# Optimization experiments

Measured on AMD Instinct MI355X. Metric: run time of the kernel, lower is better.

The kernel has to match this reference:

```python
import jax, jax.numpy as jnp
import numpy as np

B, N, D, DEG = 16, 8192, 384, 16
K, H, STEPS = 8, 128, 3


def setup_inputs() -> dict:
    key = jax.random.key(0)
    ks = jax.random.split(key, 8)
    s_in = 1.0 / np.sqrt(2 * D)
    s_h = 1.0 / np.sqrt(H)
    return {
        "q_embs": jax.random.normal(ks[0], (B, D), jnp.float32),
        "emb": jax.random.normal(ks[1], (B, N, D), jnp.float32),
        "neighbors": jax.random.randint(ks[2], (B, N, DEG), 0, N, jnp.int32),
        "labels": jax.random.randint(ks[3], (B, N), 0, 2, jnp.int32),
        "W1": jax.random.normal(ks[4], (2 * D, H), jnp.float32) * s_in,
        "b1": jnp.zeros((H,), jnp.float32),
        "W2": jax.random.normal(ks[5], (H, K), jnp.float32) * s_h,
        "b2": jnp.zeros((K,), jnp.float32),
        "P1": jax.random.normal(ks[6], (2 * D, H), jnp.float32) * s_in,
        "pb1": jnp.zeros((H,), jnp.float32),
        "P2": jax.random.normal(ks[7], (H, 1), jnp.float32) * s_h,
        "pb2": jnp.zeros((1,), jnp.float32),
    }


def reference(q_embs, emb, neighbors, labels, W1, b1, W2, b2, P1, pb1, P2, pb2):
    b, n, d = emb.shape
    k = W2.shape[1]
    # inp = [emb | q broadcast]  -> [B, N, 2D]
    inp = jnp.concatenate([emb, jnp.broadcast_to(q_embs[:, None, :], emb.shape)], axis=-1)
    # path_net: sigmoid(MLP) -> [B, N], then +1 at support (label==1) nodes
    path = jax.nn.sigmoid(jax.nn.relu(inp @ P1 + pb1) @ P2 + pb2)[..., 0]
    path = path + labels.astype(path.dtype)
    # coin_net amplitudes scaled by (1 + path)
    amps = (jax.nn.relu(inp @ W1 + b1) @ W2 + b2) * (1.0 + path)[..., None]  # [B,N,K]
    # initial uniform state
    state = jnp.full((b, n, k), 1.0 / np.sqrt(n * k), dtype=emb.dtype)

    # sparse adjacency diffusion: out[i] = sum_{j in nbrs[i]} st[j]
    spmm = jax.vmap(lambda st, nb: st[nb].sum(axis=1))  # st [N,K], nb [N,DEG]

    for _ in range(STEPS):
        st = spmm(state * amps, neighbors)                 # [B,N,K]
        norm = jnp.linalg.norm(st.reshape(b, -1), axis=1)[:, None, None]
        state = jnp.where(norm > 0, st / norm, st)
    return jnp.abs(state).sum(axis=-1)  # [B,N]
```

## Files before the change

kernel.cpp:

```cpp
#include <hip/hip_runtime.h>
#include <cstdint>
#include <cstddef>

#define BB 16
#define NN 8192
#define DD 384
#define HH 128
#define KK 8
#define DEG 16

typedef short bf8_t __attribute__((ext_vector_type(8)));
typedef float f4_t __attribute__((ext_vector_type(4)));

__device__ __forceinline__ unsigned short f2bf(float f) {
  unsigned int u = __float_as_uint(f);
  u += 0x7FFFu + ((u >> 16) & 1u);
  return (unsigned short)(u >> 16);
}

__global__ __launch_bounds__(256) void kprep(
    const float* __restrict__ q, const float* __restrict__ W1,
    const float* __restrict__ b1, const float* __restrict__ P1,
    const float* __restrict__ pb1,
    unsigned short* __restrict__ W1t, unsigned short* __restrict__ P1t,
    float* __restrict__ base1, float* __restrict__ baseP,
    float* __restrict__ normsq)
{
  int blk = blockIdx.x, t = threadIdx.x;
  if (blk < BB) {
    int net = t >> 7, h = t & 127;
    const float* W = net ? P1 : W1;
    float acc = net ? pb1[h] : b1[h];
    const float* qb = q + blk * DD;
    for (int d = 0; d < DD; ++d)
      acc = fmaf(qb[d], W[(DD + d) * HH + h], acc);
    (net ? baseP : base1)[blk * HH + h] = acc;
  } else {
    int e = (blk - BB) * 3072 + t;
    for (int it = 0; it < 12; ++it, e += 256) {
      int net = e / 49152;
      int r = e - net * 49152;
      int d = r >> 7;
      int h = r & 127;
      float v = (net ? P1 : W1)[d * HH + h];
      (net ? P1t : W1t)[h * DD + d] = f2bf(v);
    }
    if (blk == BB && t < BB) normsq[t] = 0.f;
  }
}

__global__ __launch_bounds__(256) void kmlp(
    const float* __restrict__ emb, const int* __restrict__ labels,
    const unsigned short* __restrict__ W1t, const unsigned short* __restrict__ P1t,
    const float* __restrict__ base1, const float* __restrict__ baseP,
    const float* __restrict__ W2, const float* __restrict__ b2,
    const float* __restrict__ P2, const float* __restrict__ pb2,
    float* __restrict__ amps)
{
  __shared__ __align__(16) unsigned short sA[64 * 40];
  __shared__ __align__(16) unsigned short sB1[128 * 40];
  __shared__ __align__(16) unsigned short sBP[128 * 40];
  __shared__ float sBase1[128], sBaseP[128], sW2t[8 * 128], sP2[128], sB2[8];

  const int t = threadIdx.x;
  const int b = blockIdx.x >> 7;
  const int row0 = (blockIdx.x & 127) * 64;
  const int gbase = b * NN + row0;

  if (t < 128) { sBase1[t] = base1[b * HH + t]; sP2[t] = P2[t]; }
  else         { sBaseP[t - 128] = baseP[b * HH + (t - 128)]; }
  for (int e = t; e < HH * KK; e += 256) {
    int h = e >> 3, kk = e & 7;
    sW2t[kk * 128 + h] = W2[e];
  }
  if (t < 8) sB2[t] = b2[t];

  const int w = t >> 6, lane = t & 63, q = lane >> 4, ln = lane & 15;
  f4_t zero = {0.f, 0.f, 0.f, 0.f};
  f4_t acc1[8], accP[8];
#pragma unroll
  for (int i = 0; i < 8; ++i) { acc1[i] = zero; accP[i] = zero; }

  const int ar = t >> 2;
  const int ac = (t & 3) * 8;

  for (int kc = 0; kc < DD; kc += 32) {
    {
      const float4* src = (const float4*)(emb + (size_t)(gbase + ar) * DD + kc + ac);
      float4 f0 = src[0], f1 = src[1];
      union { unsigned short us[8]; uint4 v; } pk;
      pk.us[0] = f2bf(f0.x); pk.us[1] = f2bf(f0.y);
      pk.us[2] = f2bf(f0.z); pk.us[3] = f2bf(f0.w);
      pk.us[4] = f2bf(f1.x); pk.us[5] = f2bf(f1.y);
      pk.us[6] = f2bf(f1.z); pk.us[7] = f2bf(f1.w);
      *(uint4*)&sA[ar * 40 + ac] = pk.v;
    }
#pragma unroll
    for (int rep = 0; rep < 2; ++rep) {
      int u = t + rep * 256;
      int h = u >> 2, part = u & 3;
      *(uint4*)&sB1[h * 40 + part * 8] = *(const uint4*)(W1t + h * DD + kc + part * 8);
      *(uint4*)&sBP[h * 40 + part * 8] = *(const uint4*)(P1t + h * DD + kc + part * 8);
    }
    __syncthreads();
    bf8_t af = *(const bf8_t*)&sA[(w * 16 + ln) * 40 + q * 8];
#pragma unroll
    for (int ct = 0; ct < 8; ++ct) {
      bf8_t b1f = *(const bf8_t*)&sB1[(ct * 16 + ln) * 40 + q * 8];
      acc1[ct] = __builtin_amdgcn_mfma_f32_16x16x32_bf16(af, b1f, acc1[ct], 0, 0, 0);
      bf8_t bpf = *(const bf8_t*)&sBP[(ct * 16 + ln) * 40 + q * 8];
      accP[ct] = __builtin_amdgcn_mfma_f32_16x16x32_bf16(af, bpf, accP[ct], 0, 0, 0);
    }
    __syncthreads();
  }

  const float pb2v = pb2[0];
#pragma unroll
  for (int r = 0; r < 4; ++r) {
    const int grow = row0 + w * 16 + q * 4 + r;
    float s[8];
#pragma unroll
    for (int kk = 0; kk < 8; ++kk) s[kk] = 0.f;
    float ps = 0.f;
#pragma unroll
    for (int ct = 0; ct < 8; ++ct) {
      int col = ct * 16 + ln;
      float h1 = fmaxf(acc1[ct][r] + sBase1[col], 0.f);
      float hp = fmaxf(accP[ct][r] + sBaseP[col], 0.f);
#pragma unroll
      for (int kk = 0; kk < 8; ++kk) s[kk] = fmaf(h1, sW2t[kk * 128 + col], s[kk]);
      ps = fmaf(hp, sP2[col], ps);
    }
#pragma unroll
    for (int off = 1; off < 16; off <<= 1) {
#pragma unroll
      for (int kk = 0; kk < 8; ++kk) s[kk] += __shfl_xor(s[kk], off, 64);
      ps += __shfl_xor(ps, off, 64);
    }
    if (ln == 0) {
      float path = 1.f / (1.f + __expf(-(ps + pb2v)));
      float scale = 1.f + path + (float)labels[b * NN + grow];
      float4 o0, o1;
      o0.x = (s[0] + sB2[0]) * scale; o0.y = (s[1] + sB2[1]) * scale;
      o0.z = (s[2] + sB2[2]) * scale; o0.w = (s[3] + sB2[3]) * scale;
      o1.x = (s[4] + sB2[4]) * scale; o1.y = (s[5] + sB2[5]) * scale;
      o1.z = (s[6] + sB2[6]) * scale; o1.w = (s[7] + sB2[7]) * scale;
      float4* dst = (float4*)(amps + (size_t)(b * NN + grow) * KK);
      dst[0] = o0; dst[1] = o1;
    }
  }
}

__device__ __forceinline__ void accum8(const float* __restrict__ src, int node,
                                       float4& a0, float4& a1) {
  const float4* p = (const float4*)(src + (size_t)node * KK);
  float4 v0 = p[0], v1 = p[1];
  a0.x += v0.x; a0.y += v0.y; a0.z += v0.z; a0.w += v0.w;
  a1.x += v1.x; a1.y += v1.y; a1.z += v1.z; a1.w += v1.w;
}

__device__ __forceinline__ void accum8m(const float* __restrict__ ain,
                                        const float* __restrict__ uin, int node,
                                        float4& a0, float4& a1) {
  const float4* pa = (const float4*)(ain + (size_t)node * KK);
  const float4* pu = (const float4*)(uin + (size_t)node * KK);
  float4 va0 = pa[0], va1 = pa[1], vu0 = pu[0], vu1 = pu[1];
  a0.x = fmaf(va0.x, vu0.x, a0.x); a0.y = fmaf(va0.y, vu0.y, a0.y);
  a0.z = fmaf(va0.z, vu0.z, a0.z); a0.w = fmaf(va0.w, vu0.w, a0.w);
  a1.x = fmaf(va1.x, vu1.x, a1.x); a1.y = fmaf(va1.y, vu1.y, a1.y);
  a1.z = fmaf(va1.z, vu1.z, a1.z); a1.w = fmaf(va1.w, vu1.w, a1.w);
}

__global__ __launch_bounds__(256) void sgather1(
    const int* __restrict__ nbr, const float* __restrict__ amps,
    float* __restrict__ uout)
{
  int idx = blockIdx.x * 256 + threadIdx.x;
  int base = idx & ~(NN - 1);
  const int4* nb = (const int4*)(nbr + (size_t)idx * DEG);
  float4 a0 = {0.f, 0.f, 0.f, 0.f}, a1 = {0.f, 0.f, 0.f, 0.f};
#pragma unroll
  for (int g = 0; g < 4; ++g) {
    int4 n = nb[g];
    accum8(amps, base + n.x, a0, a1);
    accum8(amps, base + n.y, a0, a1);
    accum8(amps, base + n.z, a0, a1);
    accum8(amps, base + n.w, a0, a1);
  }
  float4* dst = (float4*)(uout + (size_t)idx * KK);
  dst[0] = a0; dst[1] = a1;
}

__global__ __launch_bounds__(256) void sstep(
    const int* __restrict__ nbr, const float* __restrict__ amps,
    const float* __restrict__ uin, float* __restrict__ uout,
    float* __restrict__ normsq, int do_norm)
{
  int idx = blockIdx.x * 256 + threadIdx.x;
  int base = idx & ~(NN - 1);
  const int4* nb = (const int4*)(nbr + (size_t)idx * DEG);
  float4 a0 = {0.f, 0.f, 0.f, 0.f}, a1 = {0.f, 0.f, 0.f, 0.f};
#pragma unroll
  for (int g = 0; g < 4; ++g) {
    int4 n = nb[g];
    accum8m(amps, uin, base + n.x, a0, a1);
    accum8m(amps, uin, base + n.y, a0, a1);
    accum8m(amps, uin, base + n.z, a0, a1);
    accum8m(amps, uin, base + n.w, a0, a1);
  }
  float4* dst = (float4*)(uout + (size_t)idx * KK);
  dst[0] = a0; dst[1] = a1;
  if (do_norm) {
    float ss = a0.x * a0.x + a0.y * a0.y + a0.z * a0.z + a0.w * a0.w +
               a1.x * a1.x + a1.y * a1.y + a1.z * a1.z + a1.w * a1.w;
#pragma unroll
    for (int off = 1; off < 64; off <<= 1) ss += __shfl_xor(ss, off, 64);
    if ((threadIdx.x & 63) == 0) atomicAdd(&normsq[idx >> 13], ss);
  }
}

__global__ __launch_bounds__(256) void fout(
    const float* __restrict__ u, const float* __restrict__ normsq,
    float* __restrict__ out)
{
  int idx = blockIdx.x * 256 + threadIdx.x;
  float ns = normsq[idx >> 13];
  float inv = ns > 0.f ? rsqrtf(ns) : 1.f;
  const float4* p = (const float4*)(u + (size_t)idx * KK);
  float4 v0 = p[0], v1 = p[1];
  out[idx] = (fabsf(v0.x) + fabsf(v0.y) + fabsf(v0.z) + fabsf(v0.w) +
              fabsf(v1.x) + fabsf(v1.y) + fabsf(v1.z) + fabsf(v1.w)) * inv;
}

extern "C" void kernel_launch(void* const* d_in, const int* in_sizes, int n_in,
                              void* d_out, int out_size, void* d_ws, size_t ws_size,
                              hipStream_t stream) {
  const float* q   = (const float*)d_in[0];
  const float* emb = (const float*)d_in[1];
  const int*   nbr = (const int*)d_in[2];
  const int*   lab = (const int*)d_in[3];
  const float* W1  = (const float*)d_in[4];
  const float* b1  = (const float*)d_in[5];
  const float* W2  = (const float*)d_in[6];
  const float* b2  = (const float*)d_in[7];
  const float* P1  = (const float*)d_in[8];
  const float* pb1 = (const float*)d_in[9];
  const float* P2  = (const float*)d_in[10];
  const float* pb2 = (const float*)d_in[11];
  float* out = (float*)d_out;

  const size_t NK = (size_t)BB * NN * KK;
  float* ws     = (float*)d_ws;
  float* amps   = ws;
  float* uA     = amps + NK;
  float* uB     = uA + NK;
  float* base1  = uB + NK;
  float* baseP  = base1 + BB * HH;
  float* normsq = baseP + BB * HH;
  unsigned short* W1t = (unsigned short*)(normsq + 16);
  unsigned short* P1t = W1t + (size_t)HH * DD;

  kprep<<<48, 256, 0, stream>>>(q, W1, b1, P1, pb1, W1t, P1t, base1, baseP, normsq);
  kmlp<<<2048, 256, 0, stream>>>(emb, lab, W1t, P1t, base1, baseP, W2, b2, P2, pb2, amps);
  sgather1<<<512, 256, 0, stream>>>(nbr, amps, uA);
  sstep<<<512, 256, 0, stream>>>(nbr, amps, uA, uB, normsq, 0);
  sstep<<<512, 256, 0, stream>>>(nbr, amps, uB, uA, normsq, 1);
  fout<<<512, 256, 0, stream>>>(uA, normsq, out);
}
```

Before: 481.4 us.

## Restructure MLP GEMM loading, split kprep reduction, and fold amps multiply into gathers

The MLP kernel now loads emb straight from global into registers, prefetching the next K-chunk, instead of staging it through shared memory. The bf16 weight tiles are stored in a swizzled layout without padding, and occupancy is raised with launch bounds of 4. kprep spreads each batch/net dot product across two half-blocks with a shared reduction. The diffusion kernels now premultiply by amps at output and use two threads per node (one float4 each), which removes the second gather of amps per neighbour. Together these aim to cut gather traffic and shared-memory staging, at the cost of a more complex schedule and a register-prefetch dependence.

```diff
diff --git a/kernel.cpp b/kernel.cpp
--- a/kernel.cpp
+++ b/kernel.cpp
@@ -16,6 +16,15 @@
   unsigned int u = __float_as_uint(f);
   u += 0x7FFFu + ((u >> 16) & 1u);
   return (unsigned short)(u >> 16);
+}
+
+__device__ __forceinline__ bf8_t pack8(float4 f0, float4 f1) {
+  union { unsigned short us[8]; bf8_t v; } pk;
+  pk.us[0] = f2bf(f0.x); pk.us[1] = f2bf(f0.y);
+  pk.us[2] = f2bf(f0.z); pk.us[3] = f2bf(f0.w);
+  pk.us[4] = f2bf(f1.x); pk.us[5] = f2bf(f1.y);
+  pk.us[6] = f2bf(f1.z); pk.us[7] = f2bf(f1.w);
+  return pk.v;
 }
 
 __global__ __launch_bounds__(256) void kprep(
@@ -27,16 +36,28 @@
     float* __restrict__ normsq)
 {
   int blk = blockIdx.x, t = threadIdx.x;
-  if (blk < BB) {
-    int net = t >> 7, h = t & 127;
-    const float* W = net ? P1 : W1;
-    float acc = net ? pb1[h] : b1[h];
-    const float* qb = q + blk * DD;
-    for (int d = 0; d < DD; ++d)
-      acc = fmaf(qb[d], W[(DD + d) * HH + h], acc);
-    (net ? baseP : base1)[blk * HH + h] = acc;
+  if (blk < 32) {
+    int b = blk >> 1, net = blk & 1;
+    const float* W = (net ? P1 : W1) + (size_t)DD * HH;
+    const float* qb = q + b * DD;
+    int h = t & 127, half = t >> 7;
+    int d0 = half * 192;
+    float a0 = 0.f, a1 = 0.f, a2 = 0.f, a3 = 0.f;
+    for (int d = d0; d < d0 + 192; d += 4) {
+      a0 = fmaf(qb[d],     W[(size_t)d * HH + h],       a0);
+      a1 = fmaf(qb[d + 1], W[(size_t)(d + 1) * HH + h], a1);
+      a2 = fmaf(qb[d + 2], W[(size_t)(d + 2) * HH + h], a2);
+      a3 = fmaf(qb[d + 3], W[(size_t)(d + 3) * HH + h], a3);
+    }
+    __shared__ float red[256];
+    red[t] = (a0 + a1) + (a2 + a3);
+    __syncthreads();
+    if (t < 128) {
+      float tot = red[t] + red[t + 128] + (net ? pb1[h] : b1[h]);
+      (net ? baseP : base1)[b * HH + h] = tot;
+    }
   } else {
-    int e = (blk - BB) * 3072 + t;
+    int e = (blk - 32) * 3072 + t;
     for (int it = 0; it < 12; ++it, e += 256) {
       int net = e / 49152;
       int r = e - net * 49152;
@@ -45,11 +66,11 @@
       float v = (net ? P1 : W1)[d * HH + h];
       (net ? P1t : W1t)[h * DD + d] = f2bf(v);
     }
-    if (blk == BB && t < BB) normsq[t] = 0.f;
-  }
-}
-
-__global__ __launch_bounds__(256) void kmlp(
+    if (blk == 32 && t < BB) normsq[t] = 0.f;
+  }
+}
+
+__global__ __launch_bounds__(256, 4) void kmlp(
     const float* __restrict__ emb, const int* __restrict__ labels,
     const unsigned short* __restrict__ W1t, const unsigned short* __restrict__ P1t,
     const float* __restrict__ base1, const float* __restrict__ baseP,
@@ -57,61 +78,75 @@
     const float* __restrict__ P2, const float* __restrict__ pb2,
     float* __restrict__ amps)
 {
-  __shared__ __align__(16) unsigned short sA[64 * 40];
-  __shared__ __align__(16) unsigned short sB1[128 * 40];
-  __shared__ __align__(16) unsigned short sBP[128 * 40];
-  __shared__ float sBase1[128], sBaseP[128], sW2t[8 * 128], sP2[128], sB2[8];
+  __shared__ __align__(16) unsigned short sB[2 * 4096];
+  __shared__ float sCol[128 * 4];
+  __shared__ float sW2a[128 * 9];
+  __shared__ float sB2[8];
 
   const int t = threadIdx.x;
   const int b = blockIdx.x >> 7;
   const int row0 = (blockIdx.x & 127) * 64;
-  const int gbase = b * NN + row0;
-
-  if (t < 128) { sBase1[t] = base1[b * HH + t]; sP2[t] = P2[t]; }
-  else         { sBaseP[t - 128] = baseP[b * HH + (t - 128)]; }
+
+  if (t < 128) {
+    sCol[t * 4 + 0] = base1[b * HH + t];
+    sCol[t * 4 + 1] = baseP[b * HH + t];
+    sCol[t * 4 + 2] = P2[t];
+  }
   for (int e = t; e < HH * KK; e += 256) {
     int h = e >> 3, kk = e & 7;
-    sW2t[kk * 128 + h] = W2[e];
+    sW2a[h * 9 + kk] = W2[e];
   }
   if (t < 8) sB2[t] = b2[t];
 
   const int w = t >> 6, lane = t & 63, q = lane >> 4, ln = lane & 15;
+  const float* arow = emb + (size_t)(b * NN + row0 + w * 16 + ln) * DD + q * 8;
+
+  f4_t acc1[8], accP[8];
   f4_t zero = {0.f, 0.f, 0.f, 0.f};
-  f4_t acc1[8], accP[8];
 #pragma unroll
   for (int i = 0; i < 8; ++i) { acc1[i] = zero; accP[i] = zero; }
 
-  const int ar = t >> 2;
-  const int ac = (t & 3) * 8;
-
-  for (int kc = 0; kc < DD; kc += 32) {
-    {
-      const float4* src = (const float4*)(emb + (size_t)(gbase + ar) * DD + kc + ac);
-      float4 f0 = src[0], f1 = src[1];
-      union { unsigned short us[8]; uint4 v; } pk;
-      pk.us[0] = f2bf(f0.x); pk.us[1] = f2bf(f0.y);
-      pk.us[2] = f2bf(f0.z); pk.us[3] = f2bf(f0.w);
-      pk.us[4] = f2bf(f1.x); pk.us[5] = f2bf(f1.y);
-      pk.us[6] = f2bf(f1.z); pk.us[7] = f2bf(f1.w);
-      *(uint4*)&sA[ar * 40 + ac] = pk.v;
-    }
-#pragma unroll
-    for (int rep = 0; rep < 2; ++rep) {
-      int u = t + rep * 256;
-      int h = u >> 2, part = u & 3;
-      *(uint4*)&sB1[h * 40 + part * 8] = *(const uint4*)(W1t + h * DD + kc + part * 8);
-      *(uint4*)&sBP[h * 40 + part * 8] = *(const uint4*)(P1t + h * DD + kc + part * 8);
-    }
+  float4 a0c = ((const float4*)arow)[0];
+  float4 a1c = ((const float4*)arow)[1];
+#pragma unroll
+  for (int i = 0; i < 4; ++i) {
+    int gidx = i * 256 + t;
+    int net = gidx >> 9, rr = gidx & 511, h = rr >> 2, p = rr & 3;
+    uint4 v = *(const uint4*)((net ? P1t : W1t) + h * DD + p * 8);
+    int pos = p ^ ((h >> 1) & 3);
+    *(uint4*)&sB[net * 4096 + h * 32 + pos * 8] = v;
+  }
+
+  for (int kc = 0;;) {
     __syncthreads();
-    bf8_t af = *(const bf8_t*)&sA[(w * 16 + ln) * 40 + q * 8];
+    const int kn = kc + 32;
+    float4 a0n, a1n;
+    if (kn < DD) {
+      a0n = ((const float4*)(arow + kn))[0];
+      a1n = ((const float4*)(arow + kn))[1];
+    }
+    bf8_t af = pack8(a0c, a1c);
+    const int swz = (q ^ ((ln >> 1) & 3)) * 8;
 #pragma unroll
     for (int ct = 0; ct < 8; ++ct) {
-      bf8_t b1f = *(const bf8_t*)&sB1[(ct * 16 + ln) * 40 + q * 8];
-      acc1[ct] = __builtin_amdgcn_mfma_f32_16x16x32_bf16(af, b1f, acc1[ct], 0, 0, 0);
-      bf8_t bpf = *(const bf8_t*)&sBP[(ct * 16 + ln) * 40 + q * 8];
-      accP[ct] = __builtin_amdgcn_mfma_f32_16x16x32_bf16(af, bpf, accP[ct], 0, 0, 0);
-    }
+      const int off = (ct * 16 + ln) * 32 + swz;
+      bf8_t bf1 = *(const bf8_t*)&sB[off];
+      acc1[ct] = __builtin_amdgcn_mfma_f32_16x16x32_bf16(af, bf1, acc1[ct], 0, 0, 0);
+      bf8_t bfp = *(const bf8_t*)&sB[4096 + off];
+      accP[ct] = __builtin_amdgcn_mfma_f32_16x16x32_bf16(af, bfp, accP[ct], 0, 0, 0);
+    }
+    kc = kn;
+    if (kc >= DD) break;
     __syncthreads();
+#pragma unroll
+    for (int i = 0; i < 4; ++i) {
+      int gidx = i * 256 + t;
+      int net = gidx >> 9, rr = gidx & 511, h = rr >> 2, p = rr & 3;
+      uint4 v = *(const uint4*)((net ? P1t : W1t) + h * DD + kc + p * 8);
+      int pos = p ^ ((h >> 1) & 3);
+      *(uint4*)&sB[net * 4096 + h * 32 + pos * 8] = v;
+    }
+    a0c = a0n; a1c = a1n;
   }
 
   const float pb2v = pb2[0];
@@ -125,11 +160,11 @@
 #pragma unroll
     for (int ct = 0; ct < 8; ++ct) {
       int col = ct * 16 + ln;
-      float h1 = fmaxf(acc1[ct][r] + sBase1[col], 0.f);
-      float hp = fmaxf(accP[ct][r] + sBaseP[col], 0.f);
-#pragma unroll
-      for (int kk = 0; kk < 8; ++kk) s[kk] = fmaf(h1, sW2t[kk * 128 + col], s[kk]);
-      ps = fmaf(hp, sP2[col], ps);
+      float h1 = fmaxf(acc1[ct][r] + sCol[col * 4 + 0], 0.f);
+      float hp = fmaxf(accP[ct][r] + sCol[col * 4 + 1], 0.f);
+#pragma unroll
+      for (int kk = 0; kk < 8; ++kk) s[kk] = fmaf(h1, sW2a[col * 9 + kk], s[kk]);
+      ps = fmaf(hp, sCol[col * 4 + 2], ps);
     }
 #pragma unroll
     for (int off = 1; off < 16; off <<= 1) {
@@ -151,72 +186,60 @@
   }
 }
 
-__device__ __forceinline__ void accum8(const float* __restrict__ src, int node,
-                                       float4& a0, float4& a1) {
-  const float4* p = (const float4*)(src + (size_t)node * KK);
-  float4 v0 = p[0], v1 = p[1];
-  a0.x += v0.x; a0.y += v0.y; a0.z += v0.z; a0.w += v0.w;
-  a1.x += v1.x; a1.y += v1.y; a1.z += v1.z; a1.w += v1.w;
-}
-
-__device__ __forceinline__ void accum8m(const float* __restrict__ ain,
-                                        const float* __restrict__ uin, int node,
-                                        float4& a0, float4& a1) {
-  const float4* pa = (const float4*)(ain + (size_t)node * KK);
-  const float4* pu = (const float4*)(uin + (size_t)node * KK);
-  float4 va0 = pa[0], va1 = pa[1], vu0 = pu[0], vu1 = pu[1];
-  a0.x = fmaf(va0.x, vu0.x, a0.x); a0.y = fmaf(va0.y, vu0.y, a0.y);
-  a0.z = fmaf(va0.z, vu0.z, a0.z); a0.w = fmaf(va0.w, vu0.w, a0.w);
-  a1.x = fmaf(va1.x, vu1.x, a1.x); a1.y = fmaf(va1.y, vu1.y, a1.y);
-  a1.z = fmaf(va1.z, vu1.z, a1.z); a1.w = fmaf(va1.w, vu1.w, a1.w);
-}
-
-__global__ __launch_bounds__(256) void sgather1(
-    const int* __restrict__ nbr, const float* __restrict__ amps,
-    float* __restrict__ uout)
+__global__ __launch_bounds__(256) void sgm(
+    const int* __restrict__ nbr, const float* __restrict__ src,
+    const float* __restrict__ mult, float* __restrict__ out)
 {
   int idx = blockIdx.x * 256 + threadIdx.x;
-  int base = idx & ~(NN - 1);
-  const int4* nb = (const int4*)(nbr + (size_t)idx * DEG);
-  float4 a0 = {0.f, 0.f, 0.f, 0.f}, a1 = {0.f, 0.f, 0.f, 0.f};
+  int node = idx >> 1;
+  int off = (idx & 1) * 4;
+  int base = node & ~(NN - 1);
+  const int4* nb = (const int4*)(nbr + (size_t)node * DEG);
+  float4 a = {0.f, 0.f, 0.f, 0.f};
 #pragma unroll
   for (int g = 0; g < 4; ++g) {
     int4 n = nb[g];
-    accum8(amps, base + n.x, a0, a1);
-    accum8(amps, base + n.y, a0, a1);
-    accum8(amps, base + n.z, a0, a1);
-    accum8(amps, base + n.w, a0, a1);
-  }
-  float4* dst = (float4*)(uout + (size_t)idx * KK);
-  dst[0] = a0; dst[1] = a1;
-}
-
-__global__ __launch_bounds__(256) void sstep(
-    const int* __restrict__ nbr, const float* __restrict__ amps,
-    const float* __restrict__ uin, float* __restrict__ uout,
-    float* __restrict__ normsq, int do_norm)
+    float4 v0 = *(const float4*)(src + (size_t)(base + n.x) * KK + off);
+    float4 v1 = *(const float4*)(src + (size_t)(base + n.y) * KK + off);
+    float4 v2 = *(const float4*)(src + (size_t)(base + n.z) * KK + off);
+    float4 v3 = *(const float4*)(src + (size_t)(base + n.w) * KK + off);
+    a.x += v0.x + v1.x + v2.x + v3.x;
+    a.y += v0.y + v1.y + v2.y + v3.y;
+    a.z += v0.z + v1.z + v2.z + v3.z;
+    a.w += v0.w + v1.w + v2.w + v3.w;
+  }
+  float4 m = *(const float4*)(mult + (size_t)node * KK + off);
+  a.x *= m.x; a.y *= m.y; a.z *= m.z; a.w *= m.w;
+  *(float4*)(out + (size_t)node * KK + off) = a;
+}
+
+__global__ __launch_bounds__(256) void ss3(
+    const int* __restrict__ nbr, const float* __restrict__ src,
+    float* __restrict__ out, float* __restrict__ normsq)
 {
   int idx = blockIdx.x * 256 + threadIdx.x;
-  int base = idx & ~(NN - 1);
-  const int4* nb = (const int4*)(nbr + (size_t)idx * DEG);
-  float4 a0 = {0.f, 0.f, 0.f, 0.f}, a1 = {0.f, 0.f, 0.f, 0.f};
+  int node = idx >> 1;
+  int off = (idx & 1) * 4;
+  int base = node & ~(NN - 1);
+  const int4* nb = (const int4*)(nbr + (size_t)node * DEG);
+  float4 a = {0.f, 0.f, 0.f, 0.f};
 #pragma unroll
   for (int g = 0; g < 4; ++g) {
     int4 n = nb[g];
-    accum8m(amps, uin, base + n.x, a0, a1);
-    accum8m(amps, uin, base + n.y, a0, a1);
-    accum8m(amps, uin, base + n.z, a0, a1);
-    accum8m(amps, uin, base + n.w, a0, a1);
-  }
-  float4* dst = (float4*)(uout + (size_t)idx * KK);
-  dst[0] = a0; dst[1] = a1;
-  if (do_norm) {
-    float ss = a0.x * a0.x + a0.y * a0.y + a0.z * a0.z + a0.w * a0.w +
-               a1.x * a1.x + a1.y * a1.y + a1.z * a1.z + a1.w * a1.w;
-#pragma unroll
-    for (int off = 1; off < 64; off <<= 1) ss += __shfl_xor(ss, off, 64);
-    if ((threadIdx.x & 63) == 0) atomicAdd(&normsq[idx >> 13], ss);
-  }
+    float4 v0 = *(const float4*)(src + (size_t)(base + n.x) * KK + off);
+    float4 v1 = *(const float4*)(src + (size_t)(base + n.y) * KK + off);
+    float4 v2 = *(const float4*)(src + (size_t)(base + n.z) * KK + off);
+    float4 v3 = *(const float4*)(src + (size_t)(base + n.w) * KK + off);
+    a.x += v0.x + v1.x + v2.x + v3.x;
+    a.y += v0.y + v1.y + v2.y + v3.y;
+    a.z += v0.z + v1.z + v2.z + v3.z;
+    a.w += v0.w + v1.w + v2.w + v3.w;
+  }
+  *(float4*)(out + (size_t)node * KK + off) = a;
+  float ss = a.x * a.x + a.y * a.y + a.z * a.z + a.w * a.w;
+#pragma unroll
+  for (int o = 1; o < 64; o <<= 1) ss += __shfl_xor(ss, o, 64);
+  if ((threadIdx.x & 63) == 0) atomicAdd(&normsq[node >> 13], ss);
 }
 
 __global__ __launch_bounds__(256) void fout(
@@ -252,18 +275,18 @@
   const size_t NK = (size_t)BB * NN * KK;
   float* ws     = (float*)d_ws;
   float* amps   = ws;
-  float* uA     = amps + NK;
-  float* uB     = uA + NK;
-  float* base1  = uB + NK;
+  float* uB     = amps + NK;
+  float* uC     = uB + NK;
+  float* base1  = uC + NK;
   float* baseP  = base1 + BB * HH;
   float* normsq = baseP + BB * HH;
   unsigned short* W1t = (unsigned short*)(normsq + 16);
   unsigned short* P1t = W1t + (size_t)HH * DD;
 
-  kprep<<<48, 256, 0, stream>>>(q, W1, b1, P1, pb1, W1t, P1t, base1, baseP, normsq);
+  kprep<<<64, 256, 0, stream>>>(q, W1, b1, P1, pb1, W1t, P1t, base1, baseP, normsq);
   kmlp<<<2048, 256, 0, stream>>>(emb, lab, W1t, P1t, base1, baseP, W2, b2, P2, pb2, amps);
-  sgather1<<<512, 256, 0, stream>>>(nbr, amps, uA);
-  sstep<<<512, 256, 0, stream>>>(nbr, amps, uA, uB, normsq, 0);
-  sstep<<<512, 256, 0, stream>>>(nbr, amps, uB, uA, normsq, 1);
-  fout<<<512, 256, 0, stream>>>(uA, normsq, out);
-}
+  sgm<<<1024, 256, 0, stream>>>(nbr, amps, amps, uB);
+  sgm<<<1024, 256, 0, stream>>>(nbr, uB, amps, uC);
+  ss3<<<1024, 256, 0, stream>>>(nbr, uC, uB, normsq);
+  fout<<<512, 256, 0, stream>>>(uB, normsq, out);
+}
```

Result: faster. 437.8 us (-9.1%).
